# Performance work log

Hardware: AMD Instinct MI355X
Metric: run time of the kernel (lower is better)

Reference implementation:

```python
import jax, jax.numpy as jnp
import numpy as np

DIM = 1024
HEADS = 16
DIM_HEAD = 64
CHUNK = 64
INNER = HEADS * DIM_HEAD  # 1024


def setup_inputs() -> dict:
    key = jax.random.key(0)
    k1, k2, k3 = jax.random.split(key, 3)
    x = jax.random.normal(k1, (4, 4096, DIM), dtype=jnp.float32)
    # nn.Linear weights stored as (out, in); apply as x @ W.T
    w_qkv = jax.random.normal(k2, (INNER * 3, DIM), dtype=jnp.float32) * (DIM ** -0.5)
    w_out = jax.random.normal(k3, (DIM, INNER), dtype=jnp.float32) * (INNER ** -0.5)
    b_out = jnp.zeros((DIM,), dtype=jnp.float32)
    return {"x": x, "w_qkv": w_qkv, "w_out": w_out, "b_out": b_out}


def reference(x, w_qkv, w_out, b_out):
    b, n, _ = x.shape
    scale = DIM_HEAD ** -0.5
    qkv = jnp.einsum('bnd,ed->bne', x, w_qkv)  # (b, n, 3*inner)
    q, k, v = jnp.split(qkv, 3, axis=-1)
    nblk = n // CHUNK

    def to_blocks(t):
        # (b, n, h*d) -> (b, h, nblk, c, d)
        t = t.reshape(b, n, HEADS, DIM_HEAD).transpose(0, 2, 1, 3)
        return t.reshape(b, HEADS, nblk, CHUNK, DIM_HEAD)

    qb, kb, vb = to_blocks(q), to_blocks(k), to_blocks(v)
    scores = jnp.einsum('bhgqd,bhgkd->bhgqk', qb, kb) * scale  # block-local
    attn = jax.nn.softmax(scores, axis=-1)
    ob = jnp.einsum('bhgqk,bhgkd->bhgqd', attn, vb)
    out = ob.reshape(b, HEADS, n, DIM_HEAD).transpose(0, 2, 1, 3).reshape(b, n, INNER)
    return jnp.einsum('bne,de->bnd', out, w_out) + b_out
```

## Files before the change

kernel.cpp:

```cpp
#include <hip/hip_runtime.h>
#include <stdint.h>

typedef __attribute__((ext_vector_type(8))) short bf16x8;
typedef __attribute__((ext_vector_type(4))) float f32x4;
typedef __attribute__((ext_vector_type(16))) float f32x16;

__device__ __forceinline__ unsigned short bf16_of(float f) {
  union { float f; uint32_t u; } x; x.f = f;
  uint32_t r = x.u + 0x7fffu + ((x.u >> 16) & 1u);
  return (unsigned short)(r >> 16);
}

#define GLD16(gp, lp) __builtin_amdgcn_global_load_lds( \
    (const __attribute__((address_space(1))) uint32_t*)(gp), \
    (__attribute__((address_space(3))) uint32_t*)(lp), 16, 0, 0)

#define BAR() do { asm volatile("" ::: "memory"); __builtin_amdgcn_s_barrier(); asm volatile("" ::: "memory"); } while (0)

__global__ void cvt_f32_bf16(const float* __restrict__ src,
                             unsigned short* __restrict__ dst, int n4) {
  int i = blockIdx.x * blockDim.x + threadIdx.x;
  int stride = gridDim.x * blockDim.x;
  for (int j = i; j < n4; j += stride) {
    float4 f = ((const float4*)src)[j];
    union { unsigned short s[4]; uint2 v; } u;
    u.s[0] = bf16_of(f.x); u.s[1] = bf16_of(f.y);
    u.s[2] = bf16_of(f.z); u.s[3] = bf16_of(f.w);
    ((uint2*)dst)[j] = u.v;
  }
}

template<int BIAS, int OUTF32, int GW, int NSEG>
__global__ __launch_bounds__(512, 2)
void gemm256g(const unsigned short* __restrict__ A,
              const unsigned short* __restrict__ B,
              void* __restrict__ C, const float* __restrict__ bias,
              int N, int K)
{
  __shared__ __align__(1024) unsigned short sm[65536];
  char* const smb = (char*)sm;
  const int tid = threadIdx.x, w = tid >> 6, lane = tid & 63;
  const int wm = w >> 2, wn = w & 3;
  const int lane31 = lane & 31, l5 = lane >> 5;
  const int srow = lane >> 3, sslot = lane & 7;
  const int cXcd = blockIdx.x & 7, iIdx = blockIdx.x >> 3;
  const int NT_tot = NSEG * 16;

  auto tileMN = [&](int s, int& mt, int& nt) {
    const int T = cXcd * (32 * NSEG) + s * 32 + iIdx;
    const int g = T / (64 * GW), rr = T % (64 * GW);
    mt = rr / GW; nt = g * GW + rr % GW;
  };

  int stOff[2][2];
  #pragma unroll
  for (int h = 0; h < 2; ++h)
    #pragma unroll
    for (int i2 = 0; i2 < 2; ++i2)
      stOff[h][i2] = (h * 128 + (i2 * 8 + w) * 8 + srow) * K + (sslot ^ srow) * 8;

  int curMt, curNt, nxtMt, nxtNt;
  tileMN(0, curMt, curNt);
  nxtMt = curMt; nxtNt = curNt;
  if (NSEG > 1) tileMN(1, nxtMt, nxtNt);
  const unsigned short* aSeg  = A + ((size_t)curMt << 8) * K;
  const unsigned short* bSeg  = B + ((size_t)curNt << 8) * K;
  const unsigned short* aSegN = A + ((size_t)nxtMt << 8) * K;
  const unsigned short* bSegN = B + ((size_t)nxtNt << 8) * K;

  auto STAGEh = [&](const unsigned short* src, int opnd, int half, int parity) {
    char* region = smb + opnd * 65536 + parity * 32768 + half * 16384;
    GLD16(src + stOff[half][0], region + w * 1024);
    GLD16(src + stOff[half][1], region + (8 + w) * 1024);
  };
  auto LDA32 = [&](char* Ab, int j, int ks) -> bf16x8 {
    const int r = 64 * j + 32 * wm + lane31;
    return *(const bf16x8*)(Ab + r * 128 + ((ks * 32 + l5 * 16) ^ ((r & 7) << 4)));
  };
  auto LDB32 = [&](char* Bb, int l, int ks) -> bf16x8 {
    const int r = 128 * l + 32 * wn + lane31;
    return *(const bf16x8*)(Bb + r * 128 + ((ks * 32 + l5 * 16) ^ ((r & 7) << 4)));
  };

  f32x16 acc[4][2] = {};

  STAGEh(bSeg, 1, 0, 0);
  STAGEh(aSeg, 0, 0, 0);
  STAGEh(bSeg, 1, 1, 0);
  STAGEh(aSeg, 0, 1, 0);

  for (int s = 0; s < NSEG; ++s) {
    for (int tt = 0; tt < 16; ++tt) {
      const int T = s * 16 + tt;
      char* Ab = smb + (T & 1) * 32768;
      char* Bb = smb + 65536 + (T & 1) * 32768;

      asm volatile("s_waitcnt vmcnt(2)" ::: "memory");
      BAR();

      if (T + 1 < NT_tot) {
        const int p1 = (T + 1) & 1;
        const unsigned short *aS, *bS;
        if (tt < 15) { aS = aSeg + ((tt + 1) << 6); bS = bSeg + ((tt + 1) << 6); }
        else         { aS = aSegN;                  bS = bSegN; }
        STAGEh(bS, 1, 0, p1);
        STAGEh(aS, 0, 0, p1);
        STAGEh(bS, 1, 1, p1);
        STAGEh(aS, 0, 1, p1);
      }

      bf16x8 a[2][4], bb0[4], bb1[4];
      #pragma unroll
      for (int ks = 0; ks < 4; ++ks) bb0[ks] = LDB32(Bb, 0, ks);
      #pragma unroll
      for (int j = 0; j < 2; ++j)
        #pragma unroll
        for (int ks = 0; ks < 4; ++ks) a[j][ks] = LDA32(Ab, j, ks);
      #pragma unroll
      for (int ks = 0; ks < 4; ++ks) bb1[ks] = LDB32(Bb, 1, ks);

      __builtin_amdgcn_s_setprio(1);
      #pragma unroll
      for (int j = 0; j < 2; ++j)
        #pragma unroll
        for (int ks = 0; ks < 4; ++ks)
          acc[j][0] = __builtin_amdgcn_mfma_f32_32x32x16_bf16(a[j][ks], bb0[ks], acc[j][0], 0, 0, 0);
      #pragma unroll
      for (int j = 0; j < 2; ++j)
        #pragma unroll
        for (int ks = 0; ks < 4; ++ks)
          acc[j][1] = __builtin_amdgcn_mfma_f32_32x32x16_bf16(a[j][ks], bb1[ks], acc[j][1], 0, 0, 0);
      __builtin_amdgcn_s_setprio(0);

      if (T + 1 < NT_tot) asm volatile("s_waitcnt vmcnt(8)" ::: "memory");
      else                asm volatile("s_waitcnt vmcnt(0)" ::: "memory");
      BAR();

      #pragma unroll
      for (int j = 0; j < 2; ++j)
        #pragma unroll
        for (int ks = 0; ks < 4; ++ks) a[j][ks] = LDA32(Ab, j + 2, ks);

      __builtin_amdgcn_s_setprio(1);
      #pragma unroll
      for (int j = 0; j < 2; ++j)
        #pragma unroll
        for (int ks = 0; ks < 4; ++ks)
          acc[j + 2][1] = __builtin_amdgcn_mfma_f32_32x32x16_bf16(a[j][ks], bb1[ks], acc[j + 2][1], 0, 0, 0);
      #pragma unroll
      for (int j = 0; j < 2; ++j)
        #pragma unroll
        for (int ks = 0; ks < 4; ++ks)
          acc[j + 2][0] = __builtin_amdgcn_mfma_f32_32x32x16_bf16(a[j][ks], bb0[ks], acc[j + 2][0], 0, 0, 0);
      __builtin_amdgcn_s_setprio(0);
    }

    const int bm0 = curMt << 8, bn0 = curNt << 8;
    #pragma unroll
    for (int l = 0; l < 2; ++l) {
      const int col = bn0 + 128 * l + 32 * wn + lane31;
      float bb = 0.0f;
      if (BIAS && OUTF32) bb = bias[col];
      #pragma unroll
      for (int j = 0; j < 4; ++j) {
        const int row0 = bm0 + 64 * j + 32 * wm + 4 * l5;
        #pragma unroll
        for (int reg = 0; reg < 16; ++reg) {
          const int row = row0 + (reg & 3) + 8 * (reg >> 2);
          if (OUTF32)
            ((float*)C)[(size_t)row * N + col] = acc[j][l][reg] + bb;
          else
            ((unsigned short*)C)[(size_t)row * N + col] = bf16_of(acc[j][l][reg]);
        }
      }
    }
    #pragma unroll
    for (int j = 0; j < 4; ++j)
      #pragma unroll
      for (int l = 0; l < 2; ++l)
        #pragma unroll
        for (int reg = 0; reg < 16; ++reg)
          acc[j][l][reg] = 0.0f;

    curMt = nxtMt; curNt = nxtNt;
    aSeg = aSegN; bSeg = bSegN;
    if (s + 2 < NSEG) {
      tileMN(s + 2, nxtMt, nxtNt);
      aSegN = A + ((size_t)nxtMt << 8) * K;
      bSegN = B + ((size_t)nxtNt << 8) * K;
    }
  }
}

__global__ __launch_bounds__(256, 2)
void attn_block(const unsigned short* __restrict__ qkv,
                unsigned short* __restrict__ o)
{
  __shared__ __align__(1024) unsigned short Qs[64 * 64];
  __shared__ __align__(1024) unsigned short Ks[64 * 64];
  __shared__ __align__(1024) unsigned short Vt[64 * 64];
  __shared__ __align__(1024) unsigned short Ps[64 * 64];
  const int tid = threadIdx.x, w = tid >> 6, lane = tid & 63;
  const int g = blockIdx.x, h = blockIdx.y, b = blockIdx.z;
  const size_t mbase = (size_t)b * 4096 + (size_t)g * 64;
  const unsigned short* qg = qkv + mbase * 3072 + h * 64;
  const unsigned short* kgl = qkv + mbase * 3072 + 1024 + h * 64;
  const unsigned short* vg = qkv + mbase * 3072 + 2048 + h * 64;

  #pragma unroll
  for (int i = 0; i < 2; ++i) {
    const int chunk = i * 4 + w;
    const int row = chunk * 8 + (lane >> 3);
    const int c8 = (lane & 7) ^ (row & 7);
    GLD16(qg + (size_t)row * 3072 + c8 * 8, (char*)Qs + chunk * 1024);
    GLD16(kgl + (size_t)row * 3072 + c8 * 8, (char*)Ks + chunk * 1024);
  }
  #pragma unroll
  for (int i = 0; i < 2; ++i) {
    const int c = i * 256 + tid;
    const int n = c >> 3, d0 = (c & 7) * 8;
    bf16x8 v = *(const bf16x8*)(vg + (size_t)n * 3072 + d0);
    #pragma unroll
    for (int j = 0; j < 8; ++j) {
      const int d = d0 + j;
      const int bo = d * 128 + n * 2;
      *(unsigned short*)((char*)Vt + (bo ^ ((d & 7) << 4))) = (unsigned short)v[j];
    }
  }
  __syncthreads();

  const int fr = lane & 15, kg = lane >> 4;
  f32x4 s[4] = {};
  #pragma unroll
  for (int kt = 0; kt < 2; ++kt) {
    const int kb = kt * 64 + kg * 16;
    const int rq = w * 16 + fr;
    bf16x8 aq = *(const bf16x8*)((const char*)Qs + rq * 128 + (kb ^ ((rq & 7) << 4)));
    #pragma unroll
    for (int nf = 0; nf < 4; ++nf) {
      const int rk = nf * 16 + fr;
      bf16x8 bk = *(const bf16x8*)((const char*)Ks + rk * 128 + (kb ^ ((rk & 7) << 4)));
      s[nf] = __builtin_amdgcn_mfma_f32_16x16x32_bf16(aq, bk, s[nf], 0, 0, 0);
    }
  }

  const float scale = 0.125f;
  float inv[4];
  #pragma unroll
  for (int r = 0; r < 4; ++r) {
    float m0 = fmaxf(fmaxf(s[0][r], s[1][r]), fmaxf(s[2][r], s[3][r]));
    #pragma unroll
    for (int d = 1; d < 16; d <<= 1) m0 = fmaxf(m0, __shfl_xor(m0, d));
    float sum = 0.0f;
    #pragma unroll
    for (int nf = 0; nf < 4; ++nf) {
      float p = __expf((s[nf][r] - m0) * scale);
      s[nf][r] = p;
      sum += p;
    }
    #pragma unroll
    for (int d = 1; d < 16; d <<= 1) sum += __shfl_xor(sum, d);
    inv[r] = 1.0f / sum;
  }

  #pragma unroll
  for (int r = 0; r < 4; ++r) {
    const int m = w * 16 + kg * 4 + r;
    #pragma unroll
    for (int nf = 0; nf < 4; ++nf) {
      const int bo = m * 128 + (nf * 16 + fr) * 2;
      *(unsigned short*)((char*)Ps + (bo ^ ((m & 7) << 4))) = bf16_of(s[nf][r] * inv[r]);
    }
  }
  __syncthreads();

  f32x4 oa[4] = {};
  #pragma unroll
  for (int kt = 0; kt < 2; ++kt) {
    const int kb = kt * 64 + kg * 16;
    const int rp = w * 16 + fr;
    bf16x8 ap = *(const bf16x8*)((const char*)Ps + rp * 128 + (kb ^ ((rp & 7) << 4)));
    #pragma unroll
    for (int df = 0; df < 4; ++df) {
      const int rv = df * 16 + fr;
      bf16x8 bv = *(const bf16x8*)((const char*)Vt + rv * 128 + (kb ^ ((rv & 7) << 4)));
      oa[df] = __builtin_amdgcn_mfma_f32_16x16x32_bf16(ap, bv, oa[df], 0, 0, 0);
    }
  }
  #pragma unroll
  for (int df = 0; df < 4; ++df) {
    #pragma unroll
    for (int r = 0; r < 4; ++r) {
      const size_t row = mbase + w * 16 + kg * 4 + r;
      const int col = h * 64 + df * 16 + fr;
      o[row * 1024 + col] = bf16_of(oa[df][r]);
    }
  }
}

extern "C" void kernel_launch(void* const* d_in, const int* in_sizes, int n_in,
                              void* d_out, int out_size, void* d_ws, size_t ws_size,
                              hipStream_t stream) {
  const float* x     = (const float*)d_in[0];
  const float* w_qkv = (const float*)d_in[1];
  const float* w_out = (const float*)d_in[2];
  const float* b_out = (const float*)d_in[3];
  char* ws = (char*)d_ws;
  const size_t SZ_X  = (size_t)16384 * 1024 * 2;
  const size_t SZ_WQ = (size_t)3072 * 1024 * 2;
  const size_t SZ_WO = (size_t)1024 * 1024 * 2;
  unsigned short* xb  = (unsigned short*)ws;
  unsigned short* wqb = (unsigned short*)(ws + SZ_X);
  unsigned short* wob = (unsigned short*)(ws + SZ_X + SZ_WQ);
  unsigned short* qkv = (unsigned short*)(ws + SZ_X + SZ_WQ + SZ_WO);
  unsigned short* ob  = xb;

  cvt_f32_bf16<<<2048, 256, 0, stream>>>(x, xb, 16384 * 1024 / 4);
  cvt_f32_bf16<<<512, 256, 0, stream>>>(w_qkv, wqb, 3072 * 1024 / 4);
  cvt_f32_bf16<<<256, 256, 0, stream>>>(w_out, wob, 1024 * 1024 / 4);
  gemm256g<0,0,6,3><<<dim3(256), 512, 0, stream>>>(xb, wqb, qkv, nullptr, 3072, 1024);
  attn_block<<<dim3(64, 16, 4), 256, 0, stream>>>(qkv, ob);
  gemm256g<1,1,4,1><<<dim3(256), 512, 0, stream>>>(ob, wob, d_out, b_out, 1024, 1024);
}
```

Measured before the change: 205.7 us.

## Switch GEMM to 16x16x32 MFMA tiles with hoisted LDS fragment loads

Rewrites the bf16 GEMM inner loop to use 16x16x32 MFMA instructions on an 8x4 grid of 4-wide accumulators instead of the 32x32x16 instruction on a 4x2 grid. All B fragments and the first half of the A fragments are read from LDS right after the barrier, before the next tile's global-to-LDS loads are issued. This drops the mid-iteration barrier and its partial vmcnt wait, leaving a single full vmcnt(0) wait per K-step. The goal is fewer barriers and different LDS access and output-store patterns, but the full wait removes some load/compute overlap, and the smaller MFMA tiles need more LDS reads and more instructions.

```diff
diff --git a/kernel.cpp b/kernel.cpp
--- a/kernel.cpp
+++ b/kernel.cpp
@@ -3,7 +3,6 @@
 
 typedef __attribute__((ext_vector_type(8))) short bf16x8;
 typedef __attribute__((ext_vector_type(4))) float f32x4;
-typedef __attribute__((ext_vector_type(16))) float f32x16;
 
 __device__ __forceinline__ unsigned short bf16_of(float f) {
   union { float f; uint32_t u; } x; x.f = f;
@@ -32,7 +31,7 @@
 
 template<int BIAS, int OUTF32, int GW, int NSEG>
 __global__ __launch_bounds__(512, 2)
-void gemm256g(const unsigned short* __restrict__ A,
+void gemm256h(const unsigned short* __restrict__ A,
               const unsigned short* __restrict__ B,
               void* __restrict__ C, const float* __restrict__ bias,
               int N, int K)
@@ -41,7 +40,8 @@
   char* const smb = (char*)sm;
   const int tid = threadIdx.x, w = tid >> 6, lane = tid & 63;
   const int wm = w >> 2, wn = w & 3;
-  const int lane31 = lane & 31, l5 = lane >> 5;
+  const int fr = lane & 15, kg = lane >> 4;
+  const int swz = (fr & 7) << 4;
   const int srow = lane >> 3, sslot = lane & 7;
   const int cXcd = blockIdx.x & 7, iIdx = blockIdx.x >> 3;
   const int NT_tot = NSEG * 16;
@@ -73,16 +73,16 @@
     GLD16(src + stOff[half][0], region + w * 1024);
     GLD16(src + stOff[half][1], region + (8 + w) * 1024);
   };
-  auto LDA32 = [&](char* Ab, int j, int ks) -> bf16x8 {
-    const int r = 64 * j + 32 * wm + lane31;
-    return *(const bf16x8*)(Ab + r * 128 + ((ks * 32 + l5 * 16) ^ ((r & 7) << 4)));
+  auto LDA = [&](char* Ab, int j, int kk) -> bf16x8 {
+    const int r = 32 * j + 16 * wm + fr;
+    return *(const bf16x8*)(Ab + r * 128 + ((kk * 64 + kg * 16) ^ swz));
   };
-  auto LDB32 = [&](char* Bb, int l, int ks) -> bf16x8 {
-    const int r = 128 * l + 32 * wn + lane31;
-    return *(const bf16x8*)(Bb + r * 128 + ((ks * 32 + l5 * 16) ^ ((r & 7) << 4)));
+  auto LDB = [&](char* Bb, int l, int kk) -> bf16x8 {
+    const int r = 64 * l + 16 * wn + fr;
+    return *(const bf16x8*)(Bb + r * 128 + ((kk * 64 + kg * 16) ^ swz));
   };
 
-  f32x16 acc[4][2] = {};
+  f32x4 acc[8][4] = {};
 
   STAGEh(bSeg, 1, 0, 0);
   STAGEh(aSeg, 0, 0, 0);
@@ -95,8 +95,14 @@
       char* Ab = smb + (T & 1) * 32768;
       char* Bb = smb + 65536 + (T & 1) * 32768;
 
-      asm volatile("s_waitcnt vmcnt(2)" ::: "memory");
+      asm volatile("s_waitcnt vmcnt(0)" ::: "memory");
       BAR();
+
+      bf16x8 a[4][2], bb[4][2];
+      #pragma unroll
+      for (int l = 0; l < 4; ++l) { bb[l][0] = LDB(Bb, l, 0); bb[l][1] = LDB(Bb, l, 1); }
+      #pragma unroll
+      for (int j = 0; j < 4; ++j) { a[j][0] = LDA(Ab, j, 0); a[j][1] = LDA(Ab, j, 1); }
 
       if (T + 1 < NT_tot) {
         const int p1 = (T + 1) & 1;
@@ -109,78 +115,52 @@
         STAGEh(aS, 0, 1, p1);
       }
 
-      bf16x8 a[2][4], bb0[4], bb1[4];
-      #pragma unroll
-      for (int ks = 0; ks < 4; ++ks) bb0[ks] = LDB32(Bb, 0, ks);
-      #pragma unroll
-      for (int j = 0; j < 2; ++j)
+      __builtin_amdgcn_s_setprio(1);
+      #pragma unroll
+      for (int kk = 0; kk < 2; ++kk)
         #pragma unroll
-        for (int ks = 0; ks < 4; ++ks) a[j][ks] = LDA32(Ab, j, ks);
-      #pragma unroll
-      for (int ks = 0; ks < 4; ++ks) bb1[ks] = LDB32(Bb, 1, ks);
-
+        for (int j = 0; j < 4; ++j)
+          #pragma unroll
+          for (int l = 0; l < 4; ++l)
+            acc[j][l] = __builtin_amdgcn_mfma_f32_16x16x32_bf16(a[j][kk], bb[l][kk], acc[j][l], 0, 0, 0);
+      __builtin_amdgcn_s_setprio(0);
+
+      #pragma unroll
+      for (int j = 0; j < 4; ++j) { a[j][0] = LDA(Ab, j + 4, 0); a[j][1] = LDA(Ab, j + 4, 1); }
       __builtin_amdgcn_s_setprio(1);
       #pragma unroll
-      for (int j = 0; j < 2; ++j)
+      for (int kk = 0; kk < 2; ++kk)
         #pragma unroll
-        for (int ks = 0; ks < 4; ++ks)
-          acc[j][0] = __builtin_amdgcn_mfma_f32_32x32x16_bf16(a[j][ks], bb0[ks], acc[j][0], 0, 0, 0);
-      #pragma unroll
-      for (int j = 0; j < 2; ++j)
+        for (int j = 0; j < 4; ++j)
+          #pragma unroll
+          for (int l = 0; l < 4; ++l)
+            acc[j + 4][l] = __builtin_amdgcn_mfma_f32_16x16x32_bf16(a[j][kk], bb[l][kk], acc[j + 4][l], 0, 0, 0);
+      __builtin_amdgcn_s_setprio(0);
+    }
+
+    const int bm0 = curMt << 8, bn0 = curNt << 8;
+    #pragma unroll
+    for (int l = 0; l < 4; ++l) {
+      const int col = bn0 + 64 * l + 16 * wn + fr;
+      float bb2 = 0.0f;
+      if (BIAS && OUTF32) bb2 = bias[col];
+      #pragma unroll
+      for (int j = 0; j < 8; ++j) {
+        const int row0 = bm0 + 32 * j + 16 * wm + kg * 4;
         #pragma unroll
-        for (int ks = 0; ks < 4; ++ks)
-          acc[j][1] = __builtin_amdgcn_mfma_f32_32x32x16_bf16(a[j][ks], bb1[ks], acc[j][1], 0, 0, 0);
-      __builtin_amdgcn_s_setprio(0);
-
-      if (T + 1 < NT_tot) asm volatile("s_waitcnt vmcnt(8)" ::: "memory");
-      else                asm volatile("s_waitcnt vmcnt(0)" ::: "memory");
-      BAR();
-
-      #pragma unroll
-      for (int j = 0; j < 2; ++j)
-        #pragma unroll
-        for (int ks = 0; ks < 4; ++ks) a[j][ks] = LDA32(Ab, j + 2, ks);
-
-      __builtin_amdgcn_s_setprio(1);
-      #pragma unroll
-      for (int j = 0; j < 2; ++j)
-        #pragma unroll
-        for (int ks = 0; ks < 4; ++ks)
-          acc[j + 2][1] = __builtin_amdgcn_mfma_f32_32x32x16_bf16(a[j][ks], bb1[ks], acc[j + 2][1], 0, 0, 0);
-      #pragma unroll
-      for (int j = 0; j < 2; ++j)
-        #pragma unroll
-        for (int ks = 0; ks < 4; ++ks)
-          acc[j + 2][0] = __builtin_amdgcn_mfma_f32_32x32x16_bf16(a[j][ks], bb0[ks], acc[j + 2][0], 0, 0, 0);
-      __builtin_amdgcn_s_setprio(0);
-    }
-
-    const int bm0 = curMt << 8, bn0 = curNt << 8;
-    #pragma unroll
-    for (int l = 0; l < 2; ++l) {
-      const int col = bn0 + 128 * l + 32 * wn + lane31;
-      float bb = 0.0f;
-      if (BIAS && OUTF32) bb = bias[col];
-      #pragma unroll
-      for (int j = 0; j < 4; ++j) {
-        const int row0 = bm0 + 64 * j + 32 * wm + 4 * l5;
-        #pragma unroll
-        for (int reg = 0; reg < 16; ++reg) {
-          const int row = row0 + (reg & 3) + 8 * (reg >> 2);
+        for (int rr = 0; rr < 4; ++rr) {
           if (OUTF32)
-            ((float*)C)[(size_t)row * N + col] = acc[j][l][reg] + bb;
+            ((float*)C)[(size_t)(row0 + rr) * N + col] = acc[j][l][rr] + bb2;
           else
-            ((unsigned short*)C)[(size_t)row * N + col] = bf16_of(acc[j][l][reg]);
+            ((unsigned short*)C)[(size_t)(row0 + rr) * N + col] = bf16_of(acc[j][l][rr]);
         }
       }
     }
     #pragma unroll
-    for (int j = 0; j < 4; ++j)
-      #pragma unroll
-      for (int l = 0; l < 2; ++l)
-        #pragma unroll
-        for (int reg = 0; reg < 16; ++reg)
-          acc[j][l][reg] = 0.0f;
+    for (int j = 0; j < 8; ++j)
+      #pragma unroll
+      for (int l = 0; l < 4; ++l)
+        acc[j][l] = f32x4{0.f, 0.f, 0.f, 0.f};
 
     curMt = nxtMt; curNt = nxtNt;
     aSeg = aSegN; bSeg = bSegN;
@@ -318,7 +298,7 @@
   cvt_f32_bf16<<<2048, 256, 0, stream>>>(x, xb, 16384 * 1024 / 4);
   cvt_f32_bf16<<<512, 256, 0, stream>>>(w_qkv, wqb, 3072 * 1024 / 4);
   cvt_f32_bf16<<<256, 256, 0, stream>>>(w_out, wob, 1024 * 1024 / 4);
-  gemm256g<0,0,6,3><<<dim3(256), 512, 0, stream>>>(xb, wqb, qkv, nullptr, 3072, 1024);
+  gemm256h<0,0,6,3><<<dim3(256), 512, 0, stream>>>(xb, wqb, qkv, nullptr, 3072, 1024);
   attn_block<<<dim3(64, 16, 4), 256, 0, stream>>>(qkv, ob);
-  gemm256g<1,1,4,1><<<dim3(256), 512, 0, stream>>>(ob, wob, d_out, b_out, 1024, 1024);
-}
+  gemm256h<1,1,4,1><<<dim3(256), 512, 0, stream>>>(ob, wob, d_out, b_out, 1024, 1024);
+}
```

New measurement: 179.7 us. -12.7%, faster.
